# Kernel tuning notes

Measured on AMD Instinct MI355X. Metric: run time of the kernel, lower is better.

The kernel has to match this reference:

```python
import jax, jax.numpy as jnp
import numpy as np
import math

B, L, H, E = 4, 2048, 16, 64

def setup_inputs() -> dict:
    key = jax.random.key(0)
    kq, kk, kv = jax.random.split(key, 3)
    queries = jax.random.normal(kq, (B, L, H, E), dtype=jnp.float32)
    keys = jax.random.normal(kk, (B, L, H, E), dtype=jnp.float32)
    values = jax.random.normal(kv, (B, L, H, E), dtype=jnp.float32)
    return {"queries": queries, "keys": keys, "values": values}

def reference(queries, keys, values):
    # queries: [B,L,H,E], keys: [B,S,H,E], values: [B,S,H,D]
    Bq, Lq, Hq, Eq = queries.shape
    scale = 1.0 / math.sqrt(Eq)
    scores = jnp.einsum('blhe,bshe->bhls', queries, keys)  # [B,H,L,S]
    Sq = keys.shape[1]
    causal = jnp.triu(jnp.ones((Lq, Sq), dtype=bool), k=1)  # True above diagonal
    scores = jnp.where(causal[None, None], -jnp.inf, scores)
    A = jax.nn.softmax(scale * scores, axis=-1)  # dropout is identity in eval
    V = jnp.einsum('bhls,bshd->blhd', A, values)
    return V
```

## Files before the change

kernel.cpp:

```cpp
#include <hip/hip_runtime.h>
#include <hip/hip_bf16.h>

typedef __attribute__((ext_vector_type(8))) short bf16x8;
typedef __attribute__((ext_vector_type(4))) short bf16x4;
typedef __attribute__((ext_vector_type(4))) float f32x4;
typedef __attribute__((ext_vector_type(16))) float f32x16;

#define NB 4
#define NL 2048
#define NH 16
#define NE 64
#define HE (NH*NE)
#define QW 32
#define QBLK 128
#define NQT (NL/QBLK)
#define NBH 64
#define NKT 32
#define TILE_IMG 16384
#define WS_NEED ((size_t)NBH * NKT * TILE_IMG)
#define QSCALE (0.125f * 1.44269504088896340736f)

union Pfrag { unsigned u[4]; bf16x8 v; };

__device__ __forceinline__ unsigned pk2(float a, float b) {
  float2 t; t.x = a; t.y = b;
  __hip_bfloat162 hh = __float22bfloat162_rn(t);
  union { __hip_bfloat162 h; unsigned u; } v; v.h = hh;
  return v.u;
}
#if defined(__has_builtin) && __has_builtin(__builtin_amdgcn_exp2f)
__device__ __forceinline__ float fast_exp2(float x) {
  return __builtin_amdgcn_exp2f(x);
}
#else
__device__ __forceinline__ float fast_exp2(float x) { return exp2f(x); }
#endif
__device__ __forceinline__ void pswap(unsigned &a, unsigned &b) {
  auto r = __builtin_amdgcn_permlane32_swap(a, b, false, false);
  a = r[0]; b = r[1];
}
#define SWZ(row,col) ((row)*128 + ((col) ^ ((((row) ^ ((row)>>2)) & 7) << 4)))

__device__ __forceinline__ void cp16(unsigned char* lds, const unsigned char* g) {
  __builtin_amdgcn_global_load_lds(
      (const __attribute__((address_space(1))) unsigned int*)g,
      (__attribute__((address_space(3))) unsigned int*)lds, 16, 0, 0);
}

__global__ __launch_bounds__(256) void fa_stage(
    const float* __restrict__ K, const float* __restrict__ V,
    unsigned char* __restrict__ img)
{
  const int tid = threadIdx.x;
  const int bid = blockIdx.x;
  const int bh  = bid >> 5;
  const int t0  = bid & 31;
  const int h = bh & (NH-1), b = bh >> 4;
  const size_t base = ((size_t)b * NL * NH + h) * NE + (size_t)(t0 * 64) * HE;
  unsigned char* kimg = img + (size_t)(bh * NKT + t0) * TILE_IMG;
  unsigned char* vimg = kimg + 8192;
  #pragma unroll
  for (int rep = 0; rep < 2; ++rep) {
    const int idx = rep * 256 + tid;
    const int row = idx >> 3, gr = idx & 7;
    const float* kp = K + base + (size_t)row * HE + gr * 8;
    f32x4 a0 = *(const f32x4*)kp;
    f32x4 a1 = *(const f32x4*)(kp + 4);
    Pfrag w;
    w.u[0] = pk2(a0[0], a0[1]); w.u[1] = pk2(a0[2], a0[3]);
    w.u[2] = pk2(a1[0], a1[1]); w.u[3] = pk2(a1[2], a1[3]);
    *(bf16x8*)(kimg + SWZ(row, gr * 16)) = w.v;
  }
  const int trow = tid >> 4, tcol = (tid & 15) * 4, sq = trow * 4;
  f32x4 vr[4];
  #pragma unroll
  for (int i = 0; i < 4; ++i)
    vr[i] = *(const f32x4*)(V + base + (size_t)(sq + i) * HE + tcol);
  #pragma unroll
  for (int j = 0; j < 4; ++j) {
    const int er = tcol + j;
    union { unsigned u[2]; bf16x4 v; } w;
    w.u[0] = pk2(vr[0][j], vr[1][j]);
    w.u[1] = pk2(vr[2][j], vr[3][j]);
    *(bf16x4*)(vimg + SWZ(er, sq * 2)) = w.v;
  }
}

#define PACK(SC, PA0, PA1)                                                     \
      {                                                                        \
        unsigned c0 = pk2(SC[0],SC[1]),   c1 = pk2(SC[2],SC[3]);               \
        unsigned c2 = pk2(SC[4],SC[5]),   c3 = pk2(SC[6],SC[7]);               \
        unsigned c4 = pk2(SC[8],SC[9]),   c5 = pk2(SC[10],SC[11]);             \
        unsigned c6 = pk2(SC[12],SC[13]), c7 = pk2(SC[14],SC[15]);             \
        pswap(c0, c2);  pswap(c1, c3);                                         \
        pswap(c4, c6);  pswap(c5, c7);                                         \
        PA0.u[0]=c0; PA0.u[1]=c1; PA0.u[2]=c2; PA0.u[3]=c3;                    \
        PA1.u[0]=c4; PA1.u[1]=c5; PA1.u[2]=c6; PA1.u[3]=c7;                    \
      }

#define LSUM(SC)                                                               \
      l_run += ((((SC[0]+SC[1])+(SC[2]+SC[3]))+((SC[4]+SC[5])+(SC[6]+SC[7])))  \
             + (((SC[8]+SC[9])+(SC[10]+SC[11]))+((SC[12]+SC[13])+(SC[14]+SC[15]))));

#define SMPACK(SC, PA0, PA1)                                                   \
      _Pragma("unroll")                                                        \
      for (int r = 0; r < 16; ++r) SC[r] = fast_exp2(SC[r]);                   \
      LSUM(SC)                                                                 \
      PACK(SC, PA0, PA1)

#define PVPREV()                                                               \
    {                                                                          \
      _Pragma("unroll")                                                        \
      for (int dt = 0; dt < 2; ++dt) {                                         \
        oacc[dt] = __builtin_amdgcn_mfma_f32_32x32x16_bf16(                    \
            vv[0][dt], p00.v, oacc[dt], 0, 0, 0);                              \
        oacc[dt] = __builtin_amdgcn_mfma_f32_32x32x16_bf16(                    \
            vv[2][dt], p10.v, oacc[dt], 0, 0, 0);                              \
        oacc[dt] = __builtin_amdgcn_mfma_f32_32x32x16_bf16(                    \
            vv[1][dt], p01.v, oacc[dt], 0, 0, 0);                              \
        oacc[dt] = __builtin_amdgcn_mfma_f32_32x32x16_bf16(                    \
            vv[3][dt], p11.v, oacc[dt], 0, 0, 0);                              \
      }                                                                        \
    }

#define TILE(IT, BUF)                                                          \
    {                                                                          \
      if ((IT) > 0) PVPREV()                                                   \
      const unsigned char* kb = &k_lds[BUF][0];                                \
      const unsigned char* vbp = &v_lds[BUF][0];                               \
      const int kv0 = (IT)*64;                                                 \
      if (kv0 + 63 <= qb) {                                                    \
        f32x16 sc0 = (f32x16)0.0f, sc1 = (f32x16)0.0f;                         \
        _Pragma("unroll")                                                      \
        for (int ks = 0; ks < 4; ++ks) {                                       \
          bf16x8 af0 = *(const bf16x8*)(kb + addr4[ks]);                       \
          bf16x8 af1 = *(const bf16x8*)(kb + addr4[ks] + 4096);                \
          sc0 = __builtin_amdgcn_mfma_f32_32x32x16_bf16(af0, qf[ks], sc0,0,0,0);\
          sc1 = __builtin_amdgcn_mfma_f32_32x32x16_bf16(af1, qf[ks], sc1,0,0,0);\
        }                                                                      \
        SMPACK(sc0, p00, p01)                                                  \
        SMPACK(sc1, p10, p11)                                                  \
      } else {                                                                 \
        if (kv0 <= qb + 31) {                                                  \
          f32x16 sc = (f32x16)0.0f;                                            \
          _Pragma("unroll")                                                    \
          for (int ks = 0; ks < 4; ++ks) {                                     \
            bf16x8 af = *(const bf16x8*)(kb + addr4[ks]);                      \
            sc = __builtin_amdgcn_mfma_f32_32x32x16_bf16(af, qf[ks], sc,0,0,0);\
          }                                                                    \
          _Pragma("unroll")                                                    \
          for (int r = 0; r < 16; ++r) {                                       \
            const int kvg = kv0 + (r&3) + 8*(r>>2) + 4*hi;                     \
            sc[r] = (kvg > qg) ? 0.0f : fast_exp2(sc[r]);                      \
          }                                                                    \
          LSUM(sc)                                                             \
          PACK(sc, p00, p01)                                                   \
        } else {                                                               \
          p00.u[0]=0; p00.u[1]=0; p00.u[2]=0; p00.u[3]=0; p01 = p00;           \
        }                                                                      \
        if (kv0 + 32 <= qb + 31) {                                             \
          f32x16 sc = (f32x16)0.0f;                                            \
          _Pragma("unroll")                                                    \
          for (int ks = 0; ks < 4; ++ks) {                                     \
            bf16x8 af = *(const bf16x8*)(kb + addr4[ks] + 4096);               \
            sc = __builtin_amdgcn_mfma_f32_32x32x16_bf16(af, qf[ks], sc,0,0,0);\
          }                                                                    \
          _Pragma("unroll")                                                    \
          for (int r = 0; r < 16; ++r) {                                       \
            const int kvg = kv0 + 32 + (r&3) + 8*(r>>2) + 4*hi;                \
            sc[r] = (kvg > qg) ? 0.0f : fast_exp2(sc[r]);                      \
          }                                                                    \
          LSUM(sc)                                                             \
          PACK(sc, p10, p11)                                                   \
        } else {                                                               \
          p10.u[0]=0; p10.u[1]=0; p10.u[2]=0; p10.u[3]=0; p11 = p10;           \
        }                                                                      \
      }                                                                        \
      _Pragma("unroll")                                                        \
      for (int j = 0; j < 4; ++j) {                                            \
        vv[j][0] = *(const bf16x8*)(vbp + addr4[j]);                           \
        vv[j][1] = *(const bf16x8*)(vbp + addr4[j] + 4096);                    \
      }                                                                        \
    }

#define SUPER(T, B0, B1)                                                       \
    {                                                                          \
      asm volatile("s_waitcnt vmcnt(0) lgkmcnt(0)" ::: "memory");              \
      __builtin_amdgcn_sched_barrier(0);                                       \
      __builtin_amdgcn_s_barrier();                                            \
      __builtin_amdgcn_sched_barrier(0);                                       \
      if ((T) + 2 < nt) {                                                      \
        unsigned char* kd = &k_lds[(B0)^2][0];                                 \
        unsigned char* vd = &v_lds[(B0)^2][0];                                 \
        cp16(kd + wb,        src_pf);                                          \
        cp16(kd + 4096 + wb, src_pf + 4096);                                   \
        cp16(vd + wb,        src_pf + 8192);                                   \
        cp16(vd + 4096 + wb, src_pf + 12288);                                  \
        src_pf += TILE_IMG;                                                    \
        if ((T) + 3 < nt) {                                                    \
          unsigned char* kd2 = &k_lds[(B1)^2][0];                              \
          unsigned char* vd2 = &v_lds[(B1)^2][0];                              \
          cp16(kd2 + wb,        src_pf);                                       \
          cp16(kd2 + 4096 + wb, src_pf + 4096);                                \
          cp16(vd2 + wb,        src_pf + 8192);                                \
          cp16(vd2 + 4096 + wb, src_pf + 12288);                               \
          src_pf += TILE_IMG;                                                  \
        }                                                                      \
      }                                                                        \
      TILE((T) + 0, B0)                                                        \
      TILE((T) + 1, B1)                                                        \
    }

__global__ __launch_bounds__(256, 2) void fa_fwd(
    const float* __restrict__ Q, const unsigned char* __restrict__ img,
    float* __restrict__ O)
{
  __shared__ unsigned char k_lds[4][8192];
  __shared__ unsigned char v_lds[4][8192];

  const int tid  = threadIdx.x;
  const int lane = tid & 63;
  const int wid  = tid >> 6;
  const int hi   = lane >> 5;
  const int ln   = lane & 31;

  const int bid = blockIdx.x;
  const int bh  = bid & 63;
  const int qt  = (NQT - 1) - (bid >> 6);
  const int h   = bh & (NH-1);
  const int b   = bh >> 4;

  const size_t base = ((size_t)b * NL * NH + h) * NE;
  const float* Qb = Q + base;
  float*       Ob = O + base;
  const unsigned char* bimg = img + (size_t)bh * NKT * TILE_IMG;

  int addr4[4];
  {
    const int F = ((ln ^ (ln >> 2)) & 7) << 4;
    #pragma unroll
    for (int j = 0; j < 4; ++j) addr4[j] = ln*128 + ((j*32 + hi*16) ^ F);
  }
  const int wb = wid << 10;

  const int q0 = qt * QBLK;
  const int qb = q0 + wid * QW;
  const int nt = qt * 2 + 2;
  const int qg = qb + ln;

  bf16x8 qf[4];
  {
    const float* qp = Qb + (size_t)(qb + ln) * HE + hi * 8;
    #pragma unroll
    for (int ks = 0; ks < 4; ++ks) {
      f32x4 a0 = *(const f32x4*)(qp + ks*16);
      f32x4 a1 = *(const f32x4*)(qp + ks*16 + 4);
      Pfrag f;
      f.u[0] = pk2(a0[0]*QSCALE, a0[1]*QSCALE);
      f.u[1] = pk2(a0[2]*QSCALE, a0[3]*QSCALE);
      f.u[2] = pk2(a1[0]*QSCALE, a1[1]*QSCALE);
      f.u[3] = pk2(a1[2]*QSCALE, a1[3]*QSCALE);
      qf[ks] = f.v;
    }
  }
  f32x16 oacc[2];
  oacc[0] = (f32x16)0.0f; oacc[1] = (f32x16)0.0f;
  float l_run = 0.0f;
  Pfrag p00, p01, p10, p11;
  p00.u[0]=0;p00.u[1]=0;p00.u[2]=0;p00.u[3]=0; p01=p00; p10=p00; p11=p00;
  bf16x8 vv[4][2];

  asm volatile("s_waitcnt vmcnt(0)" ::: "memory");
  __builtin_amdgcn_sched_barrier(0);
  const unsigned char* src_pf = bimg + (size_t)tid * 16;
  cp16(&k_lds[0][0] + wb,        src_pf);
  cp16(&k_lds[0][0] + 4096 + wb, src_pf + 4096);
  cp16(&v_lds[0][0] + wb,        src_pf + 8192);
  cp16(&v_lds[0][0] + 4096 + wb, src_pf + 12288);
  src_pf += TILE_IMG;
  cp16(&k_lds[1][0] + wb,        src_pf);
  cp16(&k_lds[1][0] + 4096 + wb, src_pf + 4096);
  cp16(&v_lds[1][0] + wb,        src_pf + 8192);
  cp16(&v_lds[1][0] + 4096 + wb, src_pf + 12288);
  src_pf += TILE_IMG;

  int t0 = 0;
  #pragma unroll 1
  for (; t0 + 4 <= nt; t0 += 4) {
    SUPER(t0 + 0, 0, 1)
    SUPER(t0 + 2, 2, 3)
  }
  if (t0 < nt) SUPER(t0, 0, 1)
  PVPREV()

  const float l_tot = l_run + __shfl_xor(l_run, 32);
  const float inv = 1.0f / l_tot;
  float* op = Ob + (size_t)(qb + ln) * HE;
  #pragma unroll
  for (int dt = 0; dt < 2; ++dt)
    #pragma unroll
    for (int rq = 0; rq < 4; ++rq) {
      f32x4 w;
      w[0]=oacc[dt][rq*4+0]*inv; w[1]=oacc[dt][rq*4+1]*inv;
      w[2]=oacc[dt][rq*4+2]*inv; w[3]=oacc[dt][rq*4+3]*inv;
      *(f32x4*)(op + dt*32 + 8*rq + 4*hi) = w;
    }
}

__global__ __launch_bounds__(256, 3) void fa_fwd_fused(
    const float* __restrict__ Q, const float* __restrict__ K,
    const float* __restrict__ V, float* __restrict__ O)
{
  __shared__ unsigned char kf_lds[2][64*128];
  __shared__ unsigned char vf_lds[2][64*128];
  const int tid  = threadIdx.x;
  const int lane = tid & 63;
  const int wid  = tid >> 6;
  const int hi   = lane >> 5;
  const int ln   = lane & 31;
  const int trow = tid >> 4;
  const int tcol = (tid & 15) * 4;
  const int sq   = trow * 4;
  const int bidp = blockIdx.x;
  const int lb   = (bidp & 7) * 64 + (bidp >> 3);
  const int pair = lb & 7;
  const int bh   = lb >> 3;
  const int h    = bh & (NH-1);
  const int b    = bh >> 4;
  const size_t base = ((size_t)b * NL * NH + h) * NE;
  const float* Qb = Q + base;
  const float* Kb = K + base;
  const float* Vb = V + base;
  float*       Ob = O + base;
  int cur = 0;
  #pragma unroll 1
  for (int hf = 0; hf < 2; ++hf) {
    const int qt = hf ? (NQT - 1 - pair) : pair;
    const int q0 = qt * QBLK;
    const int qb = q0 + wid * QW;
    const int nt = qt * 2 + 2;
    const int qg = qb + ln;
    bf16x8 qf[4];
    {
      const float* qp = Qb + (size_t)(qb + ln) * HE + hi * 8;
      #pragma unroll
      for (int ks = 0; ks < 4; ++ks) {
        f32x4 a0 = *(const f32x4*)(qp + ks*16);
        f32x4 a1 = *(const f32x4*)(qp + ks*16 + 4);
        Pfrag f;
        f.u[0] = pk2(a0[0]*QSCALE, a0[1]*QSCALE);
        f.u[1] = pk2(a0[2]*QSCALE, a0[3]*QSCALE);
        f.u[2] = pk2(a1[0]*QSCALE, a1[1]*QSCALE);
        f.u[3] = pk2(a1[2]*QSCALE, a1[3]*QSCALE);
        qf[ks] = f.v;
      }
    }
    f32x16 oacc[2];
    oacc[0] = (f32x16)0.0f; oacc[1] = (f32x16)0.0f;
    float l_run = 0.0f;
    f32x4 kreg[4], vreg[4];
    #pragma unroll
    for (int p = 0; p < 4; ++p)
      kreg[p] = *(const f32x4*)(Kb + (size_t)(trow + p*16) * HE + tcol);
    #pragma unroll
    for (int i = 0; i < 4; ++i)
      vreg[i] = *(const f32x4*)(Vb + (size_t)(sq + i) * HE + tcol);
    #pragma unroll 1
    for (int it = 0; it < nt; ++it) {
      unsigned char* kb = kf_lds[cur];
      unsigned char* vb = vf_lds[cur];
      #pragma unroll
      for (int p = 0; p < 4; ++p) {
        const int row = trow + p*16;
        union { unsigned u[2]; bf16x4 v; } w;
        w.u[0] = pk2(kreg[p][0], kreg[p][1]);
        w.u[1] = pk2(kreg[p][2], kreg[p][3]);
        *(bf16x4*)(kb + SWZ(row, tcol*2)) = w.v;
      }
      #pragma unroll
      for (int j = 0; j < 4; ++j) {
        const int er = tcol + j;
        union { unsigned u[2]; bf16x4 v; } w;
        w.u[0] = pk2(vreg[0][j], vreg[1][j]);
        w.u[1] = pk2(vreg[2][j], vreg[3][j]);
        *(bf16x4*)(vb + SWZ(er, sq*2)) = w.v;
      }
      if (it + 1 < nt) {
        const int s0 = (it + 1) * 64;
        #pragma unroll
        for (int p = 0; p < 4; ++p)
          kreg[p] = *(const f32x4*)(Kb + (size_t)(s0 + trow + p*16) * HE + tcol);
        #pragma unroll
        for (int i = 0; i < 4; ++i)
          vreg[i] = *(const f32x4*)(Vb + (size_t)(s0 + sq + i) * HE + tcol);
      }
      asm volatile("s_waitcnt lgkmcnt(0)" ::: "memory");
      __builtin_amdgcn_sched_barrier(0);
      __builtin_amdgcn_s_barrier();
      __builtin_amdgcn_sched_barrier(0);
      #pragma unroll
      for (int sub = 0; sub < 2; ++sub) {
        const int kv0s = it*64 + sub*32;
        if (kv0s <= qb + QW - 1) {
          f32x16 sc = (f32x16)0.0f;
          #pragma unroll
          for (int ks = 0; ks < 4; ++ks) {
            const int kvr = sub*32 + ln;
            bf16x8 af = *(const bf16x8*)(kb + SWZ(kvr, ks*32 + hi*16));
            sc = __builtin_amdgcn_mfma_f32_32x32x16_bf16(af, qf[ks], sc, 0, 0, 0);
          }
          if (kv0s + 31 > qb) {
            #pragma unroll
            for (int r = 0; r < 16; ++r) {
              const int kvg = kv0s + (r&3) + 8*(r>>2) + 4*hi;
              sc[r] = (kvg > qg) ? 0.0f : fast_exp2(sc[r]);
            }
          } else {
            #pragma unroll
            for (int r = 0; r < 16; ++r) sc[r] = fast_exp2(sc[r]);
          }
          float s0_ = (sc[0]+sc[1])+(sc[2]+sc[3]);
          float s1_ = (sc[4]+sc[5])+(sc[6]+sc[7]);
          float s2_ = (sc[8]+sc[9])+(sc[10]+sc[11]);
          float s3_ = (sc[12]+sc[13])+(sc[14]+sc[15]);
          float ls = (s0_+s1_)+(s2_+s3_);
          ls += __shfl_xor(ls, 32);
          l_run += ls;
          unsigned c0 = pk2(sc[0],sc[1]),   c1 = pk2(sc[2],sc[3]);
          unsigned c2 = pk2(sc[4],sc[5]),   c3 = pk2(sc[6],sc[7]);
          unsigned c4 = pk2(sc[8],sc[9]),   c5 = pk2(sc[10],sc[11]);
          unsigned c6 = pk2(sc[12],sc[13]), c7 = pk2(sc[14],sc[15]);
          pswap(c0, c2);  pswap(c1, c3);
          pswap(c4, c6);  pswap(c5, c7);
          Pfrag pa0, pa1;
          pa0.u[0]=c0; pa0.u[1]=c1; pa0.u[2]=c2; pa0.u[3]=c3;
          pa1.u[0]=c4; pa1.u[1]=c5; pa1.u[2]=c6; pa1.u[3]=c7;
          #pragma unroll
          for (int dt = 0; dt < 2; ++dt) {
            const int dr = dt*32 + ln;
            #pragma unroll
            for (int ks2 = 0; ks2 < 2; ++ks2) {
              bf16x8 av = *(const bf16x8*)(vb + SWZ(dr, sub*64 + ks2*32 + hi*16));
              oacc[dt] = __builtin_amdgcn_mfma_f32_32x32x16_bf16(
                  av, ks2 ? pa1.v : pa0.v, oacc[dt], 0, 0, 0);
            }
          }
        }
      }
      cur ^= 1;
    }
    const float inv = 1.0f / l_run;
    float* op = Ob + (size_t)(qb + ln) * HE;
    #pragma unroll
    for (int dt = 0; dt < 2; ++dt)
      #pragma unroll
      for (int rq = 0; rq < 4; ++rq) {
        f32x4 w;
        w[0]=oacc[dt][rq*4+0]*inv; w[1]=oacc[dt][rq*4+1]*inv;
        w[2]=oacc[dt][rq*4+2]*inv; w[3]=oacc[dt][rq*4+3]*inv;
        *(f32x4*)(op + dt*32 + 8*rq + 4*hi) = w;
      }
  }
}

extern "C" void kernel_launch(void* const* d_in, const int* in_sizes, int n_in,
                              void* d_out, int out_size, void* d_ws, size_t ws_size,
                              hipStream_t stream) {
  const float* Q = (const float*)d_in[0];
  const float* K = (const float*)d_in[1];
  const float* V = (const float*)d_in[2];
  float* O = (float*)d_out;
  if (ws_size >= WS_NEED) {
    fa_stage<<<dim3(NBH * NKT), dim3(256), 0, stream>>>(K, V, (unsigned char*)d_ws);
    fa_fwd<<<dim3(NBH * NQT), dim3(256), 0, stream>>>(
        Q, (const unsigned char*)d_ws, O);
  } else {
    fa_fwd_fused<<<dim3(NB * NH * 8), dim3(256), 0, stream>>>(Q, K, V, O);
  }
}
```

Before: 72.99 us.

## Split attention accumulators into even/odd tile chains to break MFMA dependencies

Keeps two independent sets of output accumulators, row sums, P fragments and V fragments for even and odd key tiles, then sums them at the end. Within a SUPER step, the PV product for one chain can interleave with the QK and softmax work of the other, shortening the serial MFMA dependency chain on a single accumulator. The exp and sum loops are also regrouped so both score blocks are exponentiated before reduction. The cost is many more live registers (a second 32-float accumulator pair plus extra fragments), which could cause spills or limit occupancy at launch bounds 256,2.

After: 71.10 us. 2.6% less time.

```diff
diff --git a/kernel.cpp b/kernel.cpp
--- a/kernel.cpp
+++ b/kernel.cpp
@@ -98,34 +98,27 @@
         PA1.u[0]=c4; PA1.u[1]=c5; PA1.u[2]=c6; PA1.u[3]=c7;                    \
       }
 
-#define LSUM(SC)                                                               \
-      l_run += ((((SC[0]+SC[1])+(SC[2]+SC[3]))+((SC[4]+SC[5])+(SC[6]+SC[7])))  \
-             + (((SC[8]+SC[9])+(SC[10]+SC[11]))+((SC[12]+SC[13])+(SC[14]+SC[15]))));
-
-#define SMPACK(SC, PA0, PA1)                                                   \
-      _Pragma("unroll")                                                        \
-      for (int r = 0; r < 16; ++r) SC[r] = fast_exp2(SC[r]);                   \
-      LSUM(SC)                                                                 \
-      PACK(SC, PA0, PA1)
-
-#define PVPREV()                                                               \
+#define LSUM(LR, SC)                                                           \
+      LR += ((((SC[0]+SC[1])+(SC[2]+SC[3]))+((SC[4]+SC[5])+(SC[6]+SC[7])))     \
+          + (((SC[8]+SC[9])+(SC[10]+SC[11]))+((SC[12]+SC[13])+(SC[14]+SC[15]))));
+
+#define PVDO(OACC, P00, P01, P10, P11, VV)                                     \
     {                                                                          \
       _Pragma("unroll")                                                        \
       for (int dt = 0; dt < 2; ++dt) {                                         \
-        oacc[dt] = __builtin_amdgcn_mfma_f32_32x32x16_bf16(                    \
-            vv[0][dt], p00.v, oacc[dt], 0, 0, 0);                              \
-        oacc[dt] = __builtin_amdgcn_mfma_f32_32x32x16_bf16(                    \
-            vv[2][dt], p10.v, oacc[dt], 0, 0, 0);                              \
-        oacc[dt] = __builtin_amdgcn_mfma_f32_32x32x16_bf16(                    \
-            vv[1][dt], p01.v, oacc[dt], 0, 0, 0);                              \
-        oacc[dt] = __builtin_amdgcn_mfma_f32_32x32x16_bf16(                    \
-            vv[3][dt], p11.v, oacc[dt], 0, 0, 0);                              \
+        OACC[dt] = __builtin_amdgcn_mfma_f32_32x32x16_bf16(                    \
+            VV[0][dt], P00.v, OACC[dt], 0, 0, 0);                              \
+        OACC[dt] = __builtin_amdgcn_mfma_f32_32x32x16_bf16(                    \
+            VV[2][dt], P10.v, OACC[dt], 0, 0, 0);                              \
+        OACC[dt] = __builtin_amdgcn_mfma_f32_32x32x16_bf16(                    \
+            VV[1][dt], P01.v, OACC[dt], 0, 0, 0);                              \
+        OACC[dt] = __builtin_amdgcn_mfma_f32_32x32x16_bf16(                    \
+            VV[3][dt], P11.v, OACC[dt], 0, 0, 0);                              \
       }                                                                        \
     }
 
-#define TILE(IT, BUF)                                                          \
+#define QKSM(IT, BUF, LR, P00, P01, P10, P11, VV)                              \
     {                                                                          \
-      if ((IT) > 0) PVPREV()                                                   \
       const unsigned char* kb = &k_lds[BUF][0];                                \
       const unsigned char* vbp = &v_lds[BUF][0];                               \
       const int kv0 = (IT)*64;                                                 \
@@ -138,8 +131,14 @@
           sc0 = __builtin_amdgcn_mfma_f32_32x32x16_bf16(af0, qf[ks], sc0,0,0,0);\
           sc1 = __builtin_amdgcn_mfma_f32_32x32x16_bf16(af1, qf[ks], sc1,0,0,0);\
         }                                                                      \
-        SMPACK(sc0, p00, p01)                                                  \
-        SMPACK(sc1, p10, p11)                                                  \
+        _Pragma("unroll")                                                      \
+        for (int r = 0; r < 16; ++r) sc0[r] = fast_exp2(sc0[r]);               \
+        _Pragma("unroll")                                                      \
+        for (int r = 0; r < 16; ++r) sc1[r] = fast_exp2(sc1[r]);               \
+        LSUM(LR, sc0)                                                          \
+        LSUM(LR, sc1)                                                          \
+        PACK(sc0, P00, P01)                                                    \
+        PACK(sc1, P10, P11)                                                    \
       } else {                                                                 \
         if (kv0 <= qb + 31) {                                                  \
           f32x16 sc = (f32x16)0.0f;                                            \
@@ -153,10 +152,10 @@
             const int kvg = kv0 + (r&3) + 8*(r>>2) + 4*hi;                     \
             sc[r] = (kvg > qg) ? 0.0f : fast_exp2(sc[r]);                      \
           }                                                                    \
-          LSUM(sc)                                                             \
-          PACK(sc, p00, p01)                                                   \
+          LSUM(LR, sc)                                                         \
+          PACK(sc, P00, P01)                                                   \
         } else {                                                               \
-          p00.u[0]=0; p00.u[1]=0; p00.u[2]=0; p00.u[3]=0; p01 = p00;           \
+          P00.u[0]=0; P00.u[1]=0; P00.u[2]=0; P00.u[3]=0; P01 = P00;           \
         }                                                                      \
         if (kv0 + 32 <= qb + 31) {                                             \
           f32x16 sc = (f32x16)0.0f;                                            \
@@ -170,16 +169,16 @@
             const int kvg = kv0 + 32 + (r&3) + 8*(r>>2) + 4*hi;                \
             sc[r] = (kvg > qg) ? 0.0f : fast_exp2(sc[r]);                      \
           }                                                                    \
-          LSUM(sc)                                                             \
-          PACK(sc, p10, p11)                                                   \
+          LSUM(LR, sc)                                                         \
+          PACK(sc, P10, P11)                                                   \
         } else {                                                               \
-          p10.u[0]=0; p10.u[1]=0; p10.u[2]=0; p10.u[3]=0; p11 = p10;           \
+          P10.u[0]=0; P10.u[1]=0; P10.u[2]=0; P10.u[3]=0; P11 = P10;           \
         }                                                                      \
       }                                                                        \
       _Pragma("unroll")                                                        \
       for (int j = 0; j < 4; ++j) {                                            \
-        vv[j][0] = *(const bf16x8*)(vbp + addr4[j]);                           \
-        vv[j][1] = *(const bf16x8*)(vbp + addr4[j] + 4096);                    \
+        VV[j][0] = *(const bf16x8*)(vbp + addr4[j]);                           \
+        VV[j][1] = *(const bf16x8*)(vbp + addr4[j] + 4096);                    \
       }                                                                        \
     }
 
@@ -207,8 +206,12 @@
           src_pf += TILE_IMG;                                                  \
         }                                                                      \
       }                                                                        \
-      TILE((T) + 0, B0)                                                        \
-      TILE((T) + 1, B1)                                                        \
+                                     \
+      if ((T) > 0) PVDO(oaccE, pe00, pe01, pe10, pe11, vvE)                    \
+      QKSM((T) + 0, B0, l_runE, pe00, pe01, pe10, pe11, vvE)                   \
+              \
+      if ((T) > 0) PVDO(oaccO, po00, po01, po10, po11, vvO)                    \
+      QKSM((T) + 1, B1, l_runO, po00, po01, po10, po11, vvO)                   \
     }
 
 __global__ __launch_bounds__(256, 2) void fa_fwd(
@@ -263,12 +266,15 @@
       qf[ks] = f.v;
     }
   }
-  f32x16 oacc[2];
-  oacc[0] = (f32x16)0.0f; oacc[1] = (f32x16)0.0f;
-  float l_run = 0.0f;
-  Pfrag p00, p01, p10, p11;
-  p00.u[0]=0;p00.u[1]=0;p00.u[2]=0;p00.u[3]=0; p01=p00; p10=p00; p11=p00;
-  bf16x8 vv[4][2];
+  f32x16 oaccE[2], oaccO[2];
+  oaccE[0] = (f32x16)0.0f; oaccE[1] = (f32x16)0.0f;
+  oaccO[0] = (f32x16)0.0f; oaccO[1] = (f32x16)0.0f;
+  float l_runE = 0.0f, l_runO = 0.0f;
+  Pfrag pe00, pe01, pe10, pe11, po00, po01, po10, po11;
+  pe00.u[0]=0;pe00.u[1]=0;pe00.u[2]=0;pe00.u[3]=0;
+  pe01=pe00; pe10=pe00; pe11=pe00;
+  po00=pe00; po01=pe00; po10=pe00; po11=pe00;
+  bf16x8 vvE[4][2], vvO[4][2];
 
   asm volatile("s_waitcnt vmcnt(0)" ::: "memory");
   __builtin_amdgcn_sched_barrier(0);
@@ -291,9 +297,11 @@
     SUPER(t0 + 2, 2, 3)
   }
   if (t0 < nt) SUPER(t0, 0, 1)
-  PVPREV()
-
-  const float l_tot = l_run + __shfl_xor(l_run, 32);
+  PVDO(oaccE, pe00, pe01, pe10, pe11, vvE)
+  PVDO(oaccO, po00, po01, po10, po11, vvO)
+
+  const float l_mine = l_runE + l_runO;
+  const float l_tot = l_mine + __shfl_xor(l_mine, 32);
   const float inv = 1.0f / l_tot;
   float* op = Ob + (size_t)(qb + ln) * HE;
   #pragma unroll
@@ -301,8 +309,10 @@
     #pragma unroll
     for (int rq = 0; rq < 4; ++rq) {
       f32x4 w;
-      w[0]=oacc[dt][rq*4+0]*inv; w[1]=oacc[dt][rq*4+1]*inv;
-      w[2]=oacc[dt][rq*4+2]*inv; w[3]=oacc[dt][rq*4+3]*inv;
+      w[0]=(oaccE[dt][rq*4+0]+oaccO[dt][rq*4+0])*inv;
+      w[1]=(oaccE[dt][rq*4+1]+oaccO[dt][rq*4+1])*inv;
+      w[2]=(oaccE[dt][rq*4+2]+oaccO[dt][rq*4+2])*inv;
+      w[3]=(oaccE[dt][rq*4+3]+oaccO[dt][rq*4+3])*inv;
       *(f32x4*)(op + dt*32 + 8*rq + 4*hi) = w;
     }
 }
```
